# Performance work log

Measured on AMD Instinct MI355X. Metric: run time of the kernel, lower is better.

Reference implementation:

```python
import jax, jax.numpy as jnp
import numpy as np

B, N, F, L = 16, 1536, 128, 2   # batch, input_features, enc(=dec)_features, n_layers
SLOPE = 0.2                      # LeakyReLU alpha
NEG = -1e9                       # mask fill for softmax


def setup_inputs() -> dict:
    key = jax.random.key(0)
    ks = jax.random.split(key, 14)
    g = lambda k, shape, s=0.05: (jax.random.normal(k, shape, jnp.float32) * s)
    data = jax.random.randint(ks[0], (B, N), 0, 2)          # binary presence vector
    embed = g(ks[1], (N + 1, F)).at[0].set(0.0)              # padding_idx=0 row zeroed
    return {
        "data": data,
        "embed": embed,
        "enc_W": g(ks[2], (L, F, F)),
        "enc_a_src": g(ks[3], (L, F)),
        "enc_a_dst": g(ks[4], (L, F)),
        "param_W": g(ks[5], (F, 2 * F)),
        "param_b": g(ks[6], (2 * F,)),
        "dec_W": g(ks[7], (F, F)),
        "dec_a_src": g(ks[8], (F,)),
        "dec_a_dst": g(ks[9], (F,)),
        "out_W1": g(ks[10], (F, F)),
        "out_b1": g(ks[11], (F,)),
        "out_W2": g(ks[12], (F, 1)),
        "out_b2": g(ks[13], (1,)),
    }


def _gat(x, mask, W, a_src, a_dst):
    """Single-head graph attention over a dense boolean adjacency `mask`.
    Equivalent to sparse GAT over the clique edge list data_to_edges() builds
    (self-loops included). Rows with no edges output 0."""
    h = x @ W                                    # (n, F)
    si = h @ a_src                               # (n,)
    sj = h @ a_dst                               # (n,)
    e = jax.nn.leaky_relu(si[:, None] + sj[None, :], SLOPE)
    e = jnp.where(mask, e, NEG)
    attn = jax.nn.softmax(e, axis=-1) * mask.any(axis=-1)[:, None]
    return attn @ h                              # (n, F)


def reference(data, embed, enc_W, enc_a_src, enc_a_dst, param_W, param_b,
              dec_W, dec_a_src, dec_a_dst, out_W1, out_b1, out_W2, out_b2):
    def per_sample(g):
        d = g != 0                               # active feature nodes
        m_in = d[:, None] & d[None, :]           # input clique adjacency (N, N)
        x = embed[:-1]                           # node features = embedding rows (N, F)
        for l in range(L):                       # encoder layers (n_layers=2)
            x = jax.nn.elu(_gat(x, m_in, enc_W[l], enc_a_src[l], enc_a_dst[l]))
        # variational parameterization (eval mode: dropout=id, reparam -> mean)
        par = x @ param_W + param_b              # (N, 2F)
        mean, sigma = par[:, :F], par[:, F:]
        w = (g == 1).astype(mean.dtype)
        cnt = jnp.maximum(w.sum(), 1.0)
        kld = 0.5 * jnp.sum(w[:, None] * (jnp.exp(sigma) - sigma - 1.0 + mean ** 2)) / cnt
        # append master node (last embedding row) and decode over extended clique
        enc_full = jnp.concatenate([mean, embed[-1:]], axis=0)      # (N+1, F)
        d_ext = jnp.concatenate([d, jnp.ones((1,), bool)])
        m_out = d_ext[:, None] & d_ext[None, :]                     # (N+1, N+1)
        dec = jax.nn.relu(_gat(enc_full, m_out, dec_W, dec_a_src, dec_a_dst))
        return dec[-1], kld                      # master-node readout (F,)

    feats, klds = jax.vmap(per_sample)(data)     # (B, F), (B,)
    pred = jax.nn.relu(feats @ out_W1 + out_b1) @ out_W2 + out_b2   # (B, 1)
    return pred, jnp.sum(klds)
```

## Files before the change

kernel.cpp:

```cpp
#include <hip/hip_runtime.h>

#define BB 16
#define NN 1536
#define FF 128
#define SLOPE 0.2f
#define NS 2048
#define CH2 16
#define NCH2 96
#define TI 8
#define NPB (NN/8)
#define DCS 32
#define NDC 48
#define OG 4
#define OC (NCH2/OG)

__global__ __launch_bounds__(1024) void k_sortpre(
    const int* __restrict__ data,
    const float* __restrict__ embed, const float* __restrict__ decW,
    const float* __restrict__ aS, const float* __restrict__ aD,
    const float* __restrict__ SJb, long sStride,
    const float* __restrict__ SIr, long siStride,
    int* __restrict__ actG, int* __restrict__ cntG,
    float* __restrict__ hN, float* __restrict__ sN,
    float* __restrict__ keyG, int* __restrict__ pjG,
    float* __restrict__ ROWP)
{
  int b = blockIdx.x, t = threadIdx.x;
  if (b == BB){
    __shared__ float rs[2][2];
    if (t < FF){
      float acc = 0.f;
      for (int k=0;k<FF;++k) acc += embed[(long)NN*FF + k] * decW[k*FF + t];
      hN[t] = acc;
      float ps = acc * aS[t];
      float pd = acc * aD[t];
      #pragma unroll
      for (int o=32;o;o>>=1){ ps += __shfl_down(ps,o); pd += __shfl_down(pd,o); }
      if ((t&63)==0){ rs[0][t>>6]=ps; rs[1][t>>6]=pd; }
    }
    __syncthreads();
    if (t==0){ sN[0]=rs[0][0]+rs[0][1]; sN[1]=rs[1][0]+rs[1][1]; }
    return;
  }

  __shared__ float key[NS]; __shared__ int pj[NS];
  __shared__ float sb[NS]; __shared__ float sd[NS];
  __shared__ int cntS;
  int cnt;
  if (data != nullptr){
    __shared__ int s[256];
    const int PER = NN/256;
    int local[NN/256]; int nl = 0;
    if (t < 256){
      int base = t*PER;
      #pragma unroll
      for (int u=0; u<PER; ++u){
        if (data[b*NN + base + u] != 0) local[nl++] = base+u;
      }
      s[t]=nl;
    }
    __syncthreads();
    if (t==0){ int run=0; for (int i=0;i<256;i++){ int v=s[i]; s[i]=run; run+=v; }
               cntG[b]=run; cntS=run; }
    __syncthreads();
    if (t < 256){
      int o = s[t];
      for (int u=0; u<nl; ++u) actG[b*NN + o + u] = local[u];
    }
    __syncthreads();
    cnt = cntS;
  } else {
    cnt = cntG[b];
  }

  const float* SJ = SJb + (long)b*sStride;
  const int* act = (data != nullptr) ? actG + b*NN : nullptr;
  int NSort = 32; while (NSort < cnt) NSort <<= 1;

  for (int e=t; e<NSort; e+=1024){
    if (e<cnt){ int io = act ? act[e] : e; key[e]=SJ[io]; pj[e]=io; }
    else { key[e]=__builtin_inff(); pj[e]=0; }
  }
  __syncthreads();

  {
    float v0 = (t<NSort)? key[t] : __builtin_inff();
    int   q0 = (t<NSort)? pj[t] : 0;
    float v1 = __builtin_inff(); int q1 = 0;
    bool two = (NSort > 1024);
    if (two){ v1=key[t+1024]; q1=pj[t+1024]; }
    int kmax = (NSort < 64)? NSort : 64;
    for (int k=2; k<=kmax; k<<=1){
      for (int j=k>>1; j>0; j>>=1){
        {
          float ov=__shfl_xor(v0,j); int oq=__shfl_xor(q0,j);
          bool keepmin = (((t & k)==0) == ((t & j)==0));
          bool take = keepmin ? (ov < v0) : (ov > v0);
          if (take){ v0=ov; q0=oq; }
        }
        if (two){
          int e = t+1024;
          float ov=__shfl_xor(v1,j); int oq=__shfl_xor(q1,j);
          bool keepmin = (((e & k)==0) == ((e & j)==0));
          bool take = keepmin ? (ov < v1) : (ov > v1);
          if (take){ v1=ov; q1=oq; }
        }
      }
    }
    if (t < NSort){ key[t]=v0; pj[t]=q0; }
    if (two){ key[t+1024]=v1; pj[t+1024]=q1; }
  }
  __syncthreads();

  for (int k=128; k<=NSort; k<<=1){
    for (int j=k>>1; j>=64; j>>=1){
      for (int e=t; e<NSort; e+=1024){
        int l = e ^ j;
        if (l > e){
          bool asc = ((e & k) == 0);
          float a0=key[e], a1=key[l];
          if (asc ? (a0>a1) : (a0<a1)){
            key[e]=a1; key[l]=a0; int p=pj[e]; pj[e]=pj[l]; pj[l]=p;
          }
        }
      }
      __syncthreads();
    }
    {
      float v0=0.f, v1=0.f; int q0=0, q1=0;
      if (t < NSort){ v0=key[t]; q0=pj[t]; }
      if (NSort > 1024){ v1=key[t+1024]; q1=pj[t+1024]; }
      for (int j=32; j>0; j>>=1){
        {
          float ov=__shfl_xor(v0,j); int oq=__shfl_xor(q0,j);
          bool keepmin = (((t & k)==0) == ((t & j)==0));
          bool take = keepmin ? (ov < v0) : (ov > v0);
          if (take){ v0=ov; q0=oq; }
        }
        if (NSort > 1024){
          int e = t+1024;
          float ov=__shfl_xor(v1,j); int oq=__shfl_xor(q1,j);
          bool keepmin = (((e & k)==0) == ((e & j)==0));
          bool take = keepmin ? (ov < v1) : (ov > v1);
          if (take){ v1=ov; q1=oq; }
        }
      }
      if (t < NSort){ key[t]=v0; pj[t]=q0; }
      if (NSort > 1024){ key[t+1024]=v1; pj[t+1024]=q1; }
    }
    __syncthreads();
  }

  {
    int e0 = 2*t, e1 = 2*t+1;
    float b0=0.f,b1=0.f,d0=0.f,d1=0.f;
    if (e0 < cnt){ float kk=key[e0]; b0=__expf(kk); d0=__expf(SLOPE*kk); }
    if (e1 < cnt){ float kk=key[e1]; b1=__expf(kk); d1=__expf(SLOPE*kk); }
    float sB=b0+b1, sD=d0+d1;
    int lane = t & 63, wid = t >> 6;
    float iB=sB, iD=sD;
    #pragma unroll
    for (int o=1;o<64;o<<=1){
      float uB=__shfl_up(iB,o), uD=__shfl_up(iD,o);
      if (lane>=o){ iB+=uB; iD+=uD; }
    }
    __shared__ float wsB[16], wsD[16];
    if (lane==63){ wsB[wid]=iB; wsD[wid]=iD; }
    __syncthreads();
    float offB=0.f, offD=0.f;
    for (int w=0; w<wid; ++w){ offB+=wsB[w]; offD+=wsD[w]; }
    float exB = offB + iB - sB;
    float exD = offD + iD - sD;
    if (e0 < NSort){ sb[e0]=exB+b0;    sd[e0]=exD+d0; }
    if (e1 < NSort){ sb[e1]=exB+b0+b1; sd[e1]=exD+d0+d1; }
  }
  __syncthreads();

  {
    float TBs = sb[(cnt>0)? cnt-1 : 0];
    const float* SIrb = SIr + (data ? 0L : (long)b*siStride);
    for (int r=t; r<cnt; r+=1024){
      float si = data ? SIrb[act[r]] : SIrb[r];
      float th = -si;
      int lo=0, hi=cnt;
      while (lo<hi){ int mid=(lo+hi)>>1; if (key[mid]<=th) lo=mid+1; else hi=mid; }
      float ai=__expf(si), ci=__expf(SLOPE*si);
      float SBv = (lo>0)? sb[lo-1] : 0.f;
      float SDv = (lo>0)? sd[lo-1] : 0.f;
      float4 rp;
      rp.x=ai; rp.y=ci; rp.z = ai*(TBs-SBv)+ci*SDv; rp.w=__int_as_float(lo);
      reinterpret_cast<float4*>(ROWP)[(long)b*NN+r] = rp;
      keyG[(long)b*NN+r]=key[r]; pjG[(long)b*NN+r]=pj[r];
    }
  }
}

__global__ __launch_bounds__(128) void k_rowmm(const float* __restrict__ Xv,
    const float* __restrict__ W, const float* __restrict__ aS, const float* __restrict__ aD,
    float* __restrict__ H, float* __restrict__ SI, float* __restrict__ SJ)
{
  int r0 = blockIdx.x*8;
  int f = threadIdx.x;
  __shared__ float xs[8][FF];
  #pragma unroll
  for (int r=0;r<8;++r) xs[r][f] = Xv[(long)(r0+r)*FF + f];
  __syncthreads();
  float acc[8]={0.f,0.f,0.f,0.f,0.f,0.f,0.f,0.f};
  for (int k=0;k<FF;k+=4){
    float w0 = W[(k  )*FF + f];
    float w1 = W[(k+1)*FF + f];
    float w2 = W[(k+2)*FF + f];
    float w3 = W[(k+3)*FF + f];
    #pragma unroll
    for (int r=0;r<8;++r){
      float4 x = *reinterpret_cast<const float4*>(&xs[r][k]);
      acc[r] = fmaf(x.x,w0, fmaf(x.y,w1, fmaf(x.z,w2, fmaf(x.w,w3, acc[r]))));
    }
  }
  float as = aS[f], ad = aD[f];
  __shared__ float red[2][8][2];
  #pragma unroll
  for (int r=0;r<8;++r){
    H[(long)(r0+r)*FF + f] = acc[r];
    float ps = acc[r]*as, pd = acc[r]*ad;
    #pragma unroll
    for (int o=32;o;o>>=1){ ps += __shfl_down(ps,o); pd += __shfl_down(pd,o); }
    if ((f&63)==0){ red[0][r][f>>6]=ps; red[1][r][f>>6]=pd; }
  }
  __syncthreads();
  if (f<8){
    SI[r0+f]=red[0][f][0]+red[0][f][1]; SJ[r0+f]=red[1][f][0]+red[1][f][1];
  }
}

__global__ __launch_bounds__(128) void k_chunk(
    const float* __restrict__ keyG, const int* __restrict__ pjG,
    const int* __restrict__ cntArr,
    const float* __restrict__ Hb, long hStride,
    float* __restrict__ PP, float* __restrict__ PM)
{
  int b = blockIdx.y, c = blockIdx.x, f = threadIdx.x;
  int cnt = cntArr[b];
  int k0 = c*CH2;
  if (k0 >= cnt) return;
  int k1 = k0+CH2; if (k1 > cnt) k1 = cnt;
  int kn = k1-k0;
  const float* H = Hb + (long)b*hStride + f;
  __shared__ int pjs[CH2]; __shared__ float wbs[CH2], wds[CH2];
  if (f < CH2 && f < kn){
    float kk = keyG[(long)b*NN + k0 + f];
    pjs[f] = pjG[(long)b*NN + k0 + f];
    wbs[f] = __expf(kk);
    wds[f] = __expf(SLOPE*kk);
  }
  __syncthreads();
  float accB=0.f, accD=0.f;
  float hbuf[8];
  #pragma unroll
  for (int i=0;i<8;i++) hbuf[i] = (i<kn) ? H[(long)pjs[i]*FF] : 0.f;
  long obase = ((long)b*NN + k0)*FF + f;
  int k=0;
  for (; k+8<=kn; k+=8){
    #pragma unroll
    for (int u=0;u<8;u++){
      float hv = hbuf[u];
      int kp = k+u+8;
      hbuf[u] = (kp<kn) ? H[(long)pjs[kp]*FF] : 0.f;
      accB = fmaf(wbs[k+u], hv, accB);
      accD = fmaf(wds[k+u], hv, accD);
      PP[obase + (long)(k+u)*FF] = accB;
      PM[obase + (long)(k+u)*FF] = accD;
    }
  }
  for (; k<kn; ++k){
    float hv = H[(long)pjs[k]*FF];
    accB = fmaf(wbs[k], hv, accB);
    accD = fmaf(wds[k], hv, accD);
    PP[obase + (long)k*FF] = accB;
    PM[obase + (long)k*FF] = accD;
  }
}

__global__ __launch_bounds__(512) void k_offs(
    const float* __restrict__ PP, const float* __restrict__ PM,
    const int* __restrict__ cntArr,
    float* __restrict__ OFB, float* __restrict__ OFD)
{
  int b = blockIdx.x; int t = threadIdx.x;
  int f = t & 127, g = t >> 7;
  int cnt = cntArr[b];
  float vB[OC], vD[OC];
  #pragma unroll
  for (int i=0;i<OC;++i){
    int c = g*OC + i; int k0 = c*CH2;
    int ke = k0+CH2; if (ke>cnt) ke=cnt; ke-=1; if (ke<0) ke=0;
    float pb = PP[((long)b*NN+ke)*FF+f];
    float pm = PM[((long)b*NN+ke)*FF+f];
    bool on = (k0 < cnt);
    vB[i] = on? pb : 0.f; vD[i] = on? pm : 0.f;
  }
  float rb=0.f, rd=0.f;
  #pragma unroll
  for (int i=0;i<OC;++i){
    float tb=vB[i], td=vD[i];
    vB[i]=rb; vD[i]=rd;
    rb+=tb; rd+=td;
  }
  __shared__ float totB[OG][128], totD[OG][128];
  totB[g][f]=rb; totD[g][f]=rd;
  __syncthreads();
  float ob=0.f, od=0.f;
  #pragma unroll
  for (int q=0;q<OG;++q){ if (q<g){ ob+=totB[q][f]; od+=totD[q][f]; } }
  long base = (long)b*(NCH2+1)*FF + f;
  #pragma unroll
  for (int i=0;i<OC;++i){
    OFB[base + (long)(g*OC+i)*FF] = ob + vB[i];
    OFD[base + (long)(g*OC+i)*FF] = od + vD[i];
  }
  if (g == OG-1){
    OFB[base + (long)NCH2*FF] = ob + rb;
    OFD[base + (long)NCH2*FF] = od + rd;
  }
}

__global__ __launch_bounds__(128) void k_aggout_mm(
    const float* __restrict__ PP, const float* __restrict__ PM,
    const float* __restrict__ OFB, const float* __restrict__ OFD,
    const float* __restrict__ ROWP,
    const int* __restrict__ cntArr,
    const float* __restrict__ W, const float* __restrict__ aS, const float* __restrict__ aD,
    float* __restrict__ Hout, float* __restrict__ SIo, float* __restrict__ SJo)
{
  int b = blockIdx.y;
  int cnt = cntArr[b];
  int r0 = blockIdx.x*TI;
  if (r0 >= cnt) return;
  int f = threadIdx.x;
  __shared__ float4 srow[TI];
  __shared__ float xs2[TI][FF];
  if (f < TI){
    int r = r0+f; if (r > cnt-1) r = cnt-1;
    srow[f] = reinterpret_cast<const float4*>(ROWP)[(long)b*NN + r];
  }
  __syncthreads();
  const float* ofb = OFB + (long)b*(NCH2+1)*FF;
  const float* ofd = OFD + (long)b*(NCH2+1)*FF;
  float TB = ofb[(long)NCH2*FF + f];
  int rmax = cnt - r0; if (rmax > TI) rmax = TI;
  float pb[TI], pd[TI], ob[TI], od[TI];
  #pragma unroll
  for (int u=0;u<TI;++u){
    int k = __float_as_int(srow[u].w);
    int kc = k-1; if (kc < 0) kc = 0;
    int c = kc/CH2;
    pb[u] = PP[((long)b*NN+kc)*FF+f];
    pd[u] = PM[((long)b*NN+kc)*FF+f];
    ob[u] = ofb[(long)c*FF+f];
    od[u] = ofd[(long)c*FF+f];
  }
  #pragma unroll
  for (int u=0;u<TI;++u){
    float4 rp = srow[u];
    int k = __float_as_int(rp.w);
    bool hasP = (k > 0);
    float PB = hasP ? (pb[u]+ob[u]) : 0.f;
    float PD = hasP ? (pd[u]+od[u]) : 0.f;
    float num = rp.x*(TB-PB) + rp.y*PD;
    float v = 0.f;
    if (u < rmax){
      float o2 = num/rp.z;
      v = (o2>0.f)? o2 : (__expf(o2)-1.f);
    }
    xs2[u][f] = v;
  }
  __syncthreads();
  float acc2[TI];
  #pragma unroll
  for (int u=0;u<TI;++u) acc2[u]=0.f;
  for (int k=0;k<FF;k+=4){
    float w0 = W[(k  )*FF + f];
    float w1 = W[(k+1)*FF + f];
    float w2 = W[(k+2)*FF + f];
    float w3 = W[(k+3)*FF + f];
    #pragma unroll
    for (int u=0;u<TI;++u){
      float4 x = *reinterpret_cast<const float4*>(&xs2[u][k]);
      acc2[u] = fmaf(x.x,w0, fmaf(x.y,w1, fmaf(x.z,w2, fmaf(x.w,w3, acc2[u]))));
    }
  }
  float as = aS[f], ad = aD[f];
  __shared__ float red[2][TI][2];
  #pragma unroll
  for (int u=0;u<TI;++u){
    int rr=r0+u;
    if (rr<cnt) Hout[((long)b*NN+rr)*FF+f] = acc2[u];
    float ps = acc2[u]*as, pd2 = acc2[u]*ad;
    #pragma unroll
    for (int o=32;o;o>>=1){ ps += __shfl_down(ps,o); pd2 += __shfl_down(pd2,o); }
    if ((f&63)==0){ red[0][u][f>>6]=ps; red[1][u][f>>6]=pd2; }
  }
  __syncthreads();
  if (f < TI){
    int rr=r0+f;
    if (rr<cnt){
      SIo[(long)b*NN+rr]=red[0][f][0]+red[0][f][1];
      SJo[(long)b*NN+rr]=red[1][f][0]+red[1][f][1];
    }
  }
}

__global__ __launch_bounds__(128) void k_aggout(
    const float* __restrict__ PP, const float* __restrict__ PM,
    const float* __restrict__ OFB, const float* __restrict__ OFD,
    const float* __restrict__ ROWP,
    const int* __restrict__ cntArr, float* __restrict__ XoB)
{
  int b = blockIdx.y;
  int cnt = cntArr[b];
  int r0 = blockIdx.x*TI;
  if (r0 >= cnt) return;
  int f = threadIdx.x;
  float* xo = XoB + (long)b*NN*FF;
  __shared__ float4 srow[TI];
  if (f < TI){
    int r = r0+f; if (r > cnt-1) r = cnt-1;
    srow[f] = reinterpret_cast<const float4*>(ROWP)[(long)b*NN + r];
  }
  __syncthreads();
  const float* ofb = OFB + (long)b*(NCH2+1)*FF;
  const float* ofd = OFD + (long)b*(NCH2+1)*FF;
  float TB = ofb[(long)NCH2*FF + f];
  int rmax = cnt - r0; if (rmax > TI) rmax = TI;
  float pb[TI], pd[TI], ob[TI], od[TI];
  #pragma unroll
  for (int u=0;u<TI;++u){
    int k = __float_as_int(srow[u].w);
    int kc = k-1; if (kc < 0) kc = 0;
    int c = kc/CH2;
    pb[u] = PP[((long)b*NN+kc)*FF+f];
    pd[u] = PM[((long)b*NN+kc)*FF+f];
    ob[u] = ofb[(long)c*FF+f];
    od[u] = ofd[(long)c*FF+f];
  }
  #pragma unroll
  for (int u=0;u<TI;++u){
    if (u < rmax){
      float4 rp = srow[u];
      int k = __float_as_int(rp.w);
      bool hasP = (k > 0);
      float PB = hasP ? (pb[u]+ob[u]) : 0.f;
      float PD = hasP ? (pd[u]+od[u]) : 0.f;
      float num = rp.x*(TB-PB) + rp.y*PD;
      float o2 = num/rp.z;
      xo[(long)(r0+u)*FF + f] = (o2>0.f)? o2 : (__expf(o2)-1.f);
    }
  }
}

__global__ __launch_bounds__(256) void k_pardec(const float* __restrict__ XC,
    const float* __restrict__ pW, const float* __restrict__ pB,
    const float* __restrict__ decW, const float* __restrict__ dAd,
    float* __restrict__ KPART, float* __restrict__ H3, float* __restrict__ SJd,
    const int* __restrict__ cntArr)
{
  int b = blockIdx.y; int cnt = cntArr[b];
  int bx = blockIdx.x;
  int r0 = bx*8;
  int t = threadIdx.x;
  if (r0>=cnt){
    if (t==0) KPART[b*NPB + bx] = 0.f;
    return;
  }
  const float* X = XC + (long)b*NN*FF;
  __shared__ float xs[8][FF];
  for (int e=t; e<8*FF; e+=256){
    int r=e>>7, k=e&127; int rr=r0+r;
    xs[r][k] = (rr<cnt) ? X[(long)rr*FF+k] : 0.f;
  }
  __syncthreads();
  float acc[8]={0.f,0.f,0.f,0.f,0.f,0.f,0.f,0.f};
  for (int k=0;k<FF;++k){
    float w = pW[k*2*FF + t];
    #pragma unroll
    for (int r=0;r<8;++r) acc[r]+=xs[r][k]*w;
  }
  float bb = pB[t];
  float kacc=0.f;
  #pragma unroll
  for (int r=0;r<8;++r){
    int rr=r0+r;
    if (rr>=cnt) continue;
    float v = acc[r]+bb;
    if (t<FF) kacc += v*v;
    else kacc += __expf(v)-v-1.f;
  }
  #pragma unroll
  for (int o=32;o;o>>=1) kacc += __shfl_down(kacc,o);
  __shared__ float rw[4];
  if ((t&63)==0) rw[t>>6]=kacc;
  __syncthreads();
  if (t==0) KPART[b*NPB + bx] = rw[0]+rw[1]+rw[2]+rw[3];
  __shared__ float ms[8][FF];
  if (t < FF){
    #pragma unroll
    for (int r=0;r<8;++r){
      int rr=r0+r;
      ms[r][t] = (rr<cnt) ? acc[r]+bb : 0.f;
    }
  }
  __syncthreads();
  int h = t>>7, f = t&127;
  float a2[4]={0.f,0.f,0.f,0.f};
  for (int k=0;k<FF;++k){
    float w = decW[k*FF + f];
    #pragma unroll
    for (int u=0;u<4;++u) a2[u] += ms[h*4+u][k]*w;
  }
  float ad = dAd[f];
  __shared__ float redD[8][2];
  #pragma unroll
  for (int u=0;u<4;++u){
    int rq = h*4+u; int rr = r0+rq;
    if (rr<cnt) H3[((long)b*NN+rr)*FF+f] = a2[u];
    float pd = a2[u]*ad;
    #pragma unroll
    for (int o=32;o;o>>=1) pd += __shfl_down(pd,o);
    if ((t&63)==0) redD[rq][(t>>6)&1]=pd;
  }
  __syncthreads();
  if (t<8){
    int rr=r0+t;
    if (rr<cnt) SJd[(long)b*NN+rr]=redD[t][0]+redD[t][1];
  }
}

__global__ __launch_bounds__(128) void k_dec(const float* __restrict__ H3,
    const float* __restrict__ SJ3, const float* __restrict__ sN,
    const int* __restrict__ cntArr, float* __restrict__ DECP)
{
  int b=blockIdx.y, ch=blockIdx.x;
  int cnt=cntArr[b];
  int f=threadIdx.x;
  int r0=ch*DCS; int r1 = (r0+DCS < cnt) ? r0+DCS : cnt;
  float siN = sN[0];
  const float* H = H3 + (long)b*NN*FF;
  const float* SJ = SJ3 + (long)b*NN;
  float accV=0.f, accW=0.f;
  for (int r=r0;r<r1;++r){
    float sj=SJ[r]; float x=siN+sj;
    float e=(x>=0.f)? x : SLOPE*x;
    float w=__expf(e);
    accV += w*H[(long)r*FF+f];
    accW += w;
  }
  float* P = DECP + (long)(b*NDC+ch)*(FF+1);
  P[f]=accV;
  if (f==0) P[FF]=accW;
}

__global__ __launch_bounds__(128) void k_head(const float* __restrict__ DECP,
    const float* __restrict__ hN, const float* __restrict__ sN,
    const float* __restrict__ KPART, const int* __restrict__ cntArr,
    const float* __restrict__ W1, const float* __restrict__ b1,
    const float* __restrict__ W2, const float* __restrict__ b2,
    float* __restrict__ out)
{
  int b = blockIdx.x;
  int f = threadIdx.x;
  __shared__ float rw[2];
  if (b < BB){
    float siN=sN[0], sjN=sN[1];
    float xN=siN+sjN; float eN=(xN>=0.f)?xN:SLOPE*xN; float wN=__expf(eN);
    float num=0.f, den=0.f;
    for (int c=0;c<NDC;++c){
      const float* P = DECP + (long)(b*NDC+c)*(FF+1);
      num += P[f]; den += P[FF];
    }
    num += wN*hN[f]; den += wN;
    float v = num/den;
    __shared__ float feats[FF];
    feats[f] = (v>0.f)? v : 0.f;
    __syncthreads();
    float acc=0.f;
    for (int k=0;k<FF;k+=4){
      float w0=W1[(k  )*FF+f], w1=W1[(k+1)*FF+f], w2=W1[(k+2)*FF+f], w3=W1[(k+3)*FF+f];
      float4 x = *reinterpret_cast<const float4*>(&feats[k]);
      acc = fmaf(x.x,w0, fmaf(x.y,w1, fmaf(x.z,w2, fmaf(x.w,w3, acc))));
    }
    acc += b1[f];
    acc = (acc>0.f)? acc : 0.f;
    float p = acc*W2[f];
    #pragma unroll
    for (int o=32;o;o>>=1) p += __shfl_down(p,o);
    if ((f&63)==0) rw[f>>6]=p;
    __syncthreads();
    if (f==0) out[b] = rw[0]+rw[1]+b2[0];
  } else {
    float s=0.f;
    for (int bb=0;bb<BB;++bb){
      float part=0.f;
      for (int c=f;c<NPB;c+=128) part += KPART[bb*NPB + c];
      #pragma unroll
      for (int o=32;o;o>>=1) part += __shfl_down(part,o);
      if ((f&63)==0) rw[f>>6]=part;
      __syncthreads();
      float tot = rw[0]+rw[1];
      int c=cntArr[bb]; float cf = (c>0)? (float)c : 1.f;
      s += 0.5f*tot/cf;
      __syncthreads();
    }
    if (f==0) out[16]=s;
  }
}

extern "C" void kernel_launch(void* const* d_in, const int* in_sizes, int n_in,
                              void* d_out, int out_size, void* d_ws, size_t ws_size,
                              hipStream_t stream)
{
  const int*   data  = (const int*)d_in[0];
  const float* embed = (const float*)d_in[1];
  const float* encW  = (const float*)d_in[2];
  const float* encAs = (const float*)d_in[3];
  const float* encAd = (const float*)d_in[4];
  const float* pW    = (const float*)d_in[5];
  const float* pB    = (const float*)d_in[6];
  const float* decW  = (const float*)d_in[7];
  const float* decAs = (const float*)d_in[8];
  const float* decAd = (const float*)d_in[9];
  const float* oW1   = (const float*)d_in[10];
  const float* oB1   = (const float*)d_in[11];
  const float* oW2   = (const float*)d_in[12];
  const float* oB2   = (const float*)d_in[13];
  float* out = (float*)d_out;

  float* w = (float*)d_ws;
  long o = 0;
  float* H1   = w+o; o += (long)NN*FF;
  float* H2   = w+o; o += (long)BB*NN*FF;
  float* XC   = w+o; o += (long)BB*NN*FF;
  float* PP   = w+o; o += (long)BB*NN*FF;
  float* PM   = w+o; o += (long)BB*NN*FF;
  float* SI1  = w+o; o += NN;
  float* SJ1  = w+o; o += NN;
  float* SI2  = w+o; o += (long)BB*NN;
  float* SJ2  = w+o; o += (long)BB*NN;
  float* KPART= w+o; o += (long)BB*NPB;
  float* hN   = w+o; o += FF;
  float* sN   = w+o; o += 2;
  float* DECP = w+o; o += (long)BB*NDC*(FF+1);
  float* keyG = w+o; o += (long)BB*NN;
  float* OFB  = w+o; o += (long)BB*(NCH2+1)*FF;
  float* OFD  = w+o; o += (long)BB*(NCH2+1)*FF;
  o = (o+3) & ~3L;
  float* ROWP = w+o; o += (long)BB*NN*4;
  int* act = (int*)(w+o); o += (long)BB*NN;
  int* pjG = (int*)(w+o); o += (long)BB*NN;
  int* cnt = (int*)(w+o); o += BB;
  (void)in_sizes; (void)n_in; (void)out_size; (void)ws_size;

  k_rowmm<<<NN/8,128,0,stream>>>(embed, encW, encAs, encAd, H1, SI1, SJ1);
  k_sortpre<<<BB+1,1024,0,stream>>>(data, embed, decW, decAs, decAd,
      SJ1, 0L, SI1, 0L, act, cnt, hN, sN, keyG, pjG, ROWP);
  k_chunk<<<dim3(NCH2,BB),128,0,stream>>>(keyG, pjG, cnt, H1, 0L, PP, PM);
  k_offs<<<BB,512,0,stream>>>(PP, PM, cnt, OFB, OFD);
  k_aggout_mm<<<dim3(NN/TI,BB),128,0,stream>>>(PP, PM, OFB, OFD, ROWP,
      cnt, encW + FF*FF, encAs + FF, encAd + FF, H2, SI2, SJ2);
  k_sortpre<<<BB,1024,0,stream>>>(nullptr, embed, decW, decAs, decAd,
      SJ2, (long)NN, SI2, (long)NN, act, cnt, hN, sN, keyG, pjG, ROWP);
  k_chunk<<<dim3(NCH2,BB),128,0,stream>>>(keyG, pjG, cnt, H2, (long)NN*FF, PP, PM);
  k_offs<<<BB,512,0,stream>>>(PP, PM, cnt, OFB, OFD);
  k_aggout<<<dim3(NN/TI,BB),128,0,stream>>>(PP, PM, OFB, OFD, ROWP, cnt, XC);
  k_pardec<<<dim3(NPB,BB),256,0,stream>>>(XC, pW, pB, decW, decAd,
      KPART, H2 , SJ2 , cnt);
  k_dec<<<dim3(NDC,BB),128,0,stream>>>(H2 , SJ2, sN, cnt, DECP);
  k_head<<<BB+1,128,0,stream>>>(DECP, hN, sN, KPART, cnt, oW1, oB1, oW2, oB2, out);
}
```

Before: 234.5 us.

## Fuse decoder master-node attention partials into k_pardec and drop k_dec

The decoder's master-node softmax partial sums (the exp-weighted sum of h rows and the sum of weights) are now computed inside k_pardec, per 8-row block, straight from registers and shared memory. This removes the H3/SJ round trip through global memory and one kernel launch. In exchange there are now 192 partial records per batch instead of 48, so k_head does a longer serial reduction over DECP.

Result: no change. 232.7 us (-0.7%).

```diff
diff --git a/kernel.cpp b/kernel.cpp
--- a/kernel.cpp
+++ b/kernel.cpp
@@ -9,8 +9,6 @@
 #define NCH2 96
 #define TI 8
 #define NPB (NN/8)
-#define DCS 32
-#define NDC 48
 #define OG 4
 #define OC (NCH2/OG)
 
@@ -461,15 +459,18 @@
 __global__ __launch_bounds__(256) void k_pardec(const float* __restrict__ XC,
     const float* __restrict__ pW, const float* __restrict__ pB,
     const float* __restrict__ decW, const float* __restrict__ dAd,
-    float* __restrict__ KPART, float* __restrict__ H3, float* __restrict__ SJd,
+    const float* __restrict__ sN,
+    float* __restrict__ KPART, float* __restrict__ DECP,
     const int* __restrict__ cntArr)
 {
   int b = blockIdx.y; int cnt = cntArr[b];
   int bx = blockIdx.x;
   int r0 = bx*8;
   int t = threadIdx.x;
+  float* P = DECP + (long)(b*NPB + bx)*(FF+1);
   if (r0>=cnt){
     if (t==0) KPART[b*NPB + bx] = 0.f;
+    if (t<=FF) P[t] = 0.f;
     return;
   }
   const float* X = XC + (long)b*NN*FF;
@@ -521,42 +522,41 @@
   __shared__ float redD[8][2];
   #pragma unroll
   for (int u=0;u<4;++u){
-    int rq = h*4+u; int rr = r0+rq;
-    if (rr<cnt) H3[((long)b*NN+rr)*FF+f] = a2[u];
+    int rq = h*4+u;
     float pd = a2[u]*ad;
     #pragma unroll
     for (int o=32;o;o>>=1) pd += __shfl_down(pd,o);
     if ((t&63)==0) redD[rq][(t>>6)&1]=pd;
   }
   __syncthreads();
-  if (t<8){
-    int rr=r0+t;
-    if (rr<cnt) SJd[(long)b*NN+rr]=redD[t][0]+redD[t][1];
-  }
-}
-
-__global__ __launch_bounds__(128) void k_dec(const float* __restrict__ H3,
-    const float* __restrict__ SJ3, const float* __restrict__ sN,
-    const int* __restrict__ cntArr, float* __restrict__ DECP)
-{
-  int b=blockIdx.y, ch=blockIdx.x;
-  int cnt=cntArr[b];
-  int f=threadIdx.x;
-  int r0=ch*DCS; int r1 = (r0+DCS < cnt) ? r0+DCS : cnt;
   float siN = sN[0];
-  const float* H = H3 + (long)b*NN*FF;
-  const float* SJ = SJ3 + (long)b*NN;
-  float accV=0.f, accW=0.f;
-  for (int r=r0;r<r1;++r){
-    float sj=SJ[r]; float x=siN+sj;
-    float e=(x>=0.f)? x : SLOPE*x;
-    float w=__expf(e);
-    accV += w*H[(long)r*FF+f];
-    accW += w;
-  }
-  float* P = DECP + (long)(b*NDC+ch)*(FF+1);
-  P[f]=accV;
-  if (f==0) P[FF]=accW;
+  float accV = 0.f;
+  #pragma unroll
+  for (int u=0;u<4;++u){
+    int rq = h*4+u; int rr = r0+rq;
+    float sj = redD[rq][0]+redD[rq][1];
+    float x = siN + sj;
+    float e = (x>=0.f)? x : SLOPE*x;
+    float w = (rr<cnt)? __expf(e) : 0.f;
+    accV += w * a2[u];
+  }
+  __shared__ float pv[2][FF];
+  pv[h][f] = accV;
+  __syncthreads();
+  if (t < FF) P[t] = pv[0][t] + pv[1][t];
+  if (t == 0){
+    float den = 0.f;
+    #pragma unroll
+    for (int r=0;r<8;++r){
+      int rr = r0+r;
+      if (rr>=cnt) continue;
+      float sj = redD[r][0]+redD[r][1];
+      float x = siN + sj;
+      float e = (x>=0.f)? x : SLOPE*x;
+      den += __expf(e);
+    }
+    P[FF] = den;
+  }
 }
 
 __global__ __launch_bounds__(128) void k_head(const float* __restrict__ DECP,
@@ -573,8 +573,8 @@
     float siN=sN[0], sjN=sN[1];
     float xN=siN+sjN; float eN=(xN>=0.f)?xN:SLOPE*xN; float wN=__expf(eN);
     float num=0.f, den=0.f;
-    for (int c=0;c<NDC;++c){
-      const float* P = DECP + (long)(b*NDC+c)*(FF+1);
+    for (int c=0;c<NPB;++c){
+      const float* P = DECP + (long)(b*NPB+c)*(FF+1);
       num += P[f]; den += P[FF];
     }
     num += wN*hN[f]; den += wN;
@@ -648,7 +648,7 @@
   float* KPART= w+o; o += (long)BB*NPB;
   float* hN   = w+o; o += FF;
   float* sN   = w+o; o += 2;
-  float* DECP = w+o; o += (long)BB*NDC*(FF+1);
+  float* DECP = w+o; o += (long)BB*NPB*(FF+1);
   float* keyG = w+o; o += (long)BB*NN;
   float* OFB  = w+o; o += (long)BB*(NCH2+1)*FF;
   float* OFD  = w+o; o += (long)BB*(NCH2+1)*FF;
@@ -671,8 +671,7 @@
   k_chunk<<<dim3(NCH2,BB),128,0,stream>>>(keyG, pjG, cnt, H2, (long)NN*FF, PP, PM);
   k_offs<<<BB,512,0,stream>>>(PP, PM, cnt, OFB, OFD);
   k_aggout<<<dim3(NN/TI,BB),128,0,stream>>>(PP, PM, OFB, OFD, ROWP, cnt, XC);
-  k_pardec<<<dim3(NPB,BB),256,0,stream>>>(XC, pW, pB, decW, decAd,
-      KPART, H2 , SJ2 , cnt);
-  k_dec<<<dim3(NDC,BB),128,0,stream>>>(H2 , SJ2, sN, cnt, DECP);
+  k_pardec<<<dim3(NPB,BB),256,0,stream>>>(XC, pW, pB, decW, decAd, sN,
+      KPART, DECP, cnt);
   k_head<<<BB+1,128,0,stream>>>(DECP, hN, sN, KPART, cnt, oW1, oB1, oW2, oB2, out);
 }
```
